# Kernel tuning notes

Measured on AMD Instinct MI355X. Metric: run time of the kernel, lower is better.

The kernel has to match this reference:

```python
import jax, jax.numpy as jnp
import numpy as np

B, WK, HRS = 2048, 52, 8760
DT = 0.125          # Euler step in days (3-hourly), exactly representable
RANGE_PRED = 7      # forecast horizon in days


def setup_inputs() -> dict:
    key = jax.random.key(0)
    k1, k2, k3, k4 = jax.random.split(key, 4)
    # X_in: [B, weeks, 5, 1]; channel 0 = start time in days (same across batch,
    # the torch code reads X_in[0, week, 0, 0]); channels 1..4 = N,P,Z,D init.
    X_in = jax.random.uniform(k1, (B, WK, 5, 1), jnp.float32, 0.1, 3.0)
    t0 = jnp.arange(WK, dtype=jnp.float32) * 7.0
    X_in = X_in.at[:, :, 0, 0].set(jnp.broadcast_to(t0, (B, WK)))
    global_f = jax.random.uniform(k2, (B, HRS), jnp.float32)          # light forcing in [0,1]
    global_m = jax.random.uniform(k3, (B, HRS), jnp.float32) * 0.1    # mixing rate, small
    params_value = jax.random.uniform(k4, (B, 10), jnp.float32, 0.1, 1.0)
    return {"X_in": X_in, "global_f": global_f, "global_m": global_m,
            "params_value": params_value, "dt": DT, "range_pred": RANGE_PRED}


def reference(X_in, global_f, global_m, params_value, dt, range_pred):
    # Fixed multipliers from the torch code
    pv = jnp.asarray([1.0, 2.0, 0.1, 0.05, 0.1, 0.3, 0.6, 0.15, 0.4, 0.1], X_in.dtype)
    Q0, Vm, thr = 8.0, 1.0, 0.01  # Q0 = 4 + 2.5 + 1.5 + 0
    chi, rho, gam, lam, eps, alp, bet, eta, phi, zet = [params_value[:, i][:, None] for i in range(10)]  # [B,1]

    n_steps = int(round(range_pred / dt))      # 56
    stride = int(round(1.0 / dt))              # 8 -> daily sampling of output

    # Hourly forcing gather: same time axis for every batch element (torch uses X_in[0,...])
    t0 = X_in[0, :, 0, 0]                                                     # [W]
    times = t0[:, None] + jnp.arange(n_steps + 1, dtype=X_in.dtype) * dt      # [W, S]
    idx = jnp.round(times * 24.0).astype(jnp.int32)
    f = jnp.take(global_f, idx, axis=1)[:, :, :n_steps]                       # [B, W, T]
    m = jnp.take(global_m, idx, axis=1)[:, :, :n_steps]

    def step(carry, ft_mt):
        N, P, Z, D = carry                      # each [B, W]
        ft, mt = ft_mt
        Pc = jnp.maximum(thr, P)
        Zc = jnp.maximum(thr, Z)
        gN = N / (chi * pv[0] + N)
        zg = rho * pv[1] * (1.0 - jnp.exp(-lam * pv[3] * Pc)) * Zc
        up = Vm * gN * ft * Pc
        Nn = N + dt * (-up + alp * pv[5] * zg + eps * pv[4] * P + gam * pv[2] * Z + phi * pv[8] * D + mt * (Q0 - N))
        Pn = P + dt * (up - zg - eps * pv[4] * P - eta * pv[7] * P - mt * P)
        Zn = Z + dt * (bet * pv[6] * zg - gam * pv[2] * Z - mt * Z)
        Dn = D + dt * (eta * pv[7] * P + (1.0 - alp * pv[5] - bet * pv[6]) * zg - phi * pv[8] * D - zet * pv[9] * D - mt * D)
        new = (Nn, Pn, Zn, Dn)
        return new, jnp.stack(new, axis=0)      # [4, B, W]

    carry0 = (X_in[:, :, 1, 0], X_in[:, :, 2, 0], X_in[:, :, 3, 0], X_in[:, :, 4, 0])
    _, ys = jax.lax.scan(step, carry0, (jnp.moveaxis(f, 2, 0), jnp.moveaxis(m, 2, 0)))  # ys: [T, 4, B, W]
    traj = jnp.concatenate([jnp.stack(carry0, axis=0)[None], ys], axis=0)               # [S, 4, B, W]
    out = jnp.moveaxis(traj, (0, 1), (3, 2))                                            # [B, W, 4, S]
    return out[:, :, :, ::stride]               # daily samples: [B, W, 4, range_pred+1]
```

## Files before the change

kernel.cpp:

```cpp
#include <hip/hip_runtime.h>


typedef float f32x4 __attribute__((ext_vector_type(4)));

#define NPZD_B 2048
#define NPZD_WK 52
#define NPZD_HRS 8760
#define NPZD_NF4 2190
#define NPZD_WSTRIDE 60
#define NPZD_LDSW (NPZD_WK * NPZD_WSTRIDE + 16)

__global__ __launch_bounds__(64, 4) void npzd_kernel(
    const float* __restrict__ X_in,
    const float* __restrict__ gf,
    const float* __restrict__ gm,
    const float* __restrict__ params,
    const float* __restrict__ dt_ptr,
    float* __restrict__ out)
{
    __shared__ __align__(16) float lds_f[NPZD_LDSW];
    __shared__ __align__(16) float lds_m[NPZD_LDSW];

    const int b    = blockIdx.x;
    const int lane = threadIdx.x;

    const float dt = dt_ptr[0];
    const int wc = (lane < NPZD_WK) ? lane : (NPZD_WK - 1);
    const float* xb = X_in + ((size_t)b * NPZD_WK + wc) * 5;
    const float x1 = xb[1], x2 = xb[2], x3 = xb[3], x4 = xb[4];

    const float* pp = params + (size_t)b * 10;
    const float chi   = pp[0];
    const float rho2  = pp[1] * 2.0f;
    const float gam1  = pp[2] * 0.1f;
    const float lam05 = pp[3] * 0.05f;
    const float eps1  = pp[4] * 0.1f;
    const float alp3  = pp[5] * 0.3f;
    const float bet6  = pp[6] * 0.6f;
    const float eta15 = pp[7] * 0.15f;
    const float phi4  = pp[8] * 0.4f;
    const float zet1  = pp[9] * 0.1f;
    const float rem   = 1.0f - alp3 - bet6;

    const f32x4* __restrict__ gf4 = (const f32x4*)(gf + (size_t)b * NPZD_HRS);
    const f32x4* __restrict__ gm4 = (const f32x4*)(gm + (size_t)b * NPZD_HRS);

    #pragma unroll
    for (int pass = 0; pass < 4; ++pass) {
        f32x4 fv[9], mv[9];
        int kk[9];
        #pragma unroll
        for (int c = 0; c < 9; ++c) {
            int k = (pass * 9 + c) * 64 + lane;
            if (k >= NPZD_NF4) k = NPZD_NF4 - 1;
            kk[c] = k;
            fv[c] = gf4[k];
            mv[c] = gm4[k];
        }
        #pragma unroll
        for (int c = 0; c < 9; ++c) {
            const int k = kk[c];
            const float fe[4] = {fv[c].x, fv[c].y, fv[c].z, fv[c].w};
            const float me[4] = {mv[c].x, mv[c].y, mv[c].z, mv[c].w};
            const int rm = k % 3;
            const int e0 = (rm == 0) ? 0 : (3 - rm);
            const int j0 = (4 * k + e0) / 3;
            const int p0 = j0 + 4 * ((j0 * 9363) >> 19);
            lds_f[p0] = fe[e0];
            lds_m[p0] = me[e0];
            if (rm == 0) {
                const int j1 = j0 + 1;
                const int p1 = j1 + 4 * ((j1 * 9363) >> 19);
                lds_f[p1] = fe[3];
                lds_m[p1] = me[3];
            }
        }
    }
    __syncthreads();

    if (lane >= NPZD_WK) return;
    const int w = lane;

    float N = x1, P = x2, Z = x3, D = x4;

    float oN[8], oP[8], oZ[8], oD[8];
    oN[0] = N; oP[0] = P; oZ[0] = Z; oD[0] = D;

    const float* lf = lds_f + w * NPZD_WSTRIDE;
    const float* lm = lds_m + w * NPZD_WSTRIDE;

    #pragma unroll
    for (int g = 0; g < 14; ++g) {
        const f32x4 f4 = *(const f32x4*)(lf + 4 * g);
        const f32x4 m4 = *(const f32x4*)(lm + 4 * g);
        const float fs[4] = {f4.x, f4.y, f4.z, f4.w};
        const float ms[4] = {m4.x, m4.y, m4.z, m4.w};
        #pragma unroll
        for (int q = 0; q < 4; ++q) {
            const float ft = fs[q], mt = ms[q];
            const float Pc = fmaxf(0.01f, P);
            const float Zc = fmaxf(0.01f, Z);
            const float gN = N * __builtin_amdgcn_rcpf(chi + N);
            const float zg = rho2 * (1.0f - __expf(-lam05 * Pc)) * Zc;
            const float up = gN * ft * Pc;
            const float Nn = N + dt * (-up + alp3 * zg + eps1 * P + gam1 * Z + phi4 * D + mt * (8.0f - N));
            const float Pn = P + dt * (up - zg - eps1 * P - eta15 * P - mt * P);
            const float Zn = Z + dt * (bet6 * zg - gam1 * Z - mt * Z);
            const float Dn = D + dt * (eta15 * P + rem * zg - phi4 * D - zet1 * D - mt * D);
            N = Nn; P = Pn; Z = Zn; D = Dn;
        }
        if (g & 1) {
            const int c = (g >> 1) + 1;
            oN[c] = N; oP[c] = P; oZ[c] = Z; oD[c] = D;
        }
    }

    f32x4* o4 = (f32x4*)(out + ((size_t)b * NPZD_WK + w) * 32);
    o4[0] = (f32x4){oN[0], oN[1], oN[2], oN[3]};
    o4[1] = (f32x4){oN[4], oN[5], oN[6], oN[7]};
    o4[2] = (f32x4){oP[0], oP[1], oP[2], oP[3]};
    o4[3] = (f32x4){oP[4], oP[5], oP[6], oP[7]};
    o4[4] = (f32x4){oZ[0], oZ[1], oZ[2], oZ[3]};
    o4[5] = (f32x4){oZ[4], oZ[5], oZ[6], oZ[7]};
    o4[6] = (f32x4){oD[0], oD[1], oD[2], oD[3]};
    o4[7] = (f32x4){oD[4], oD[5], oD[6], oD[7]};
}

extern "C" void kernel_launch(void* const* d_in, const int* in_sizes, int n_in,
                              void* d_out, int out_size, void* d_ws, size_t ws_size,
                              hipStream_t stream) {
    const float* X_in   = (const float*)d_in[0];
    const float* gf     = (const float*)d_in[1];
    const float* gm     = (const float*)d_in[2];
    const float* params = (const float*)d_in[3];
    const float* dt_ptr = (const float*)d_in[4];
    float* out = (float*)d_out;

    npzd_kernel<<<NPZD_B, 64, 0, stream>>>(X_in, gf, gm, params, dt_ptr, out);
}
```

Before: 182.8 us.

## Split batch rows across two blocks and pipeline forcing loads with integration

Each batch element is now handled by two blocks, each covering 26 weeks, which doubles the grid and halves the forcing data each block stages. Within a block, the forcing is loaded in two chunks of half-weeks, and the first chunk is integrated while the second chunk's global loads are in flight. The intent is to shrink LDS use, add parallelism, and hide memory latency behind the serial ODE steps. The cost is more blocks, an extra barrier, and only 26 of 64 lanes doing compute.

```diff
diff --git a/kernel.cpp b/kernel.cpp
--- a/kernel.cpp
+++ b/kernel.cpp
@@ -6,9 +6,11 @@
 #define NPZD_B 2048
 #define NPZD_WK 52
 #define NPZD_HRS 8760
-#define NPZD_NF4 2190
-#define NPZD_WSTRIDE 60
-#define NPZD_LDSW (NPZD_WK * NPZD_WSTRIDE + 16)
+#define NPZD_WKH 26
+#define NPZD_CS 28
+#define NPZD_F4C 21
+#define NPZD_NI 546
+#define NPZD_LDSW (NPZD_WKH * NPZD_CS)
 
 __global__ __launch_bounds__(64, 4) void npzd_kernel(
     const float* __restrict__ X_in,
@@ -21,12 +23,15 @@
     __shared__ __align__(16) float lds_f[NPZD_LDSW];
     __shared__ __align__(16) float lds_m[NPZD_LDSW];
 
-    const int b    = blockIdx.x;
+    const int bid  = blockIdx.x;
+    const int b    = bid >> 1;
+    const int hb   = bid & 1;
     const int lane = threadIdx.x;
 
     const float dt = dt_ptr[0];
-    const int wc = (lane < NPZD_WK) ? lane : (NPZD_WK - 1);
-    const float* xb = X_in + ((size_t)b * NPZD_WK + wc) * 5;
+    const int wl = (lane < NPZD_WKH) ? lane : (NPZD_WKH - 1);
+    const int wg = NPZD_WKH * hb + wl;
+    const float* xb = X_in + ((size_t)b * NPZD_WK + wg) * 5;
     const float x1 = xb[1], x2 = xb[2], x3 = xb[3], x4 = xb[4];
 
     const float* pp = params + (size_t)b * 10;
@@ -45,77 +50,82 @@
     const f32x4* __restrict__ gf4 = (const f32x4*)(gf + (size_t)b * NPZD_HRS);
     const f32x4* __restrict__ gm4 = (const f32x4*)(gm + (size_t)b * NPZD_HRS);
 
+    float N = x1, P = x2, Z = x3, D = x4;
+    float oN[8], oP[8], oZ[8], oD[8];
+    oN[0] = N; oP[0] = P; oZ[0] = Z; oD[0] = D;
+
     #pragma unroll
-    for (int pass = 0; pass < 4; ++pass) {
+    for (int c = 0; c < 2; ++c) {
         f32x4 fv[9], mv[9];
-        int kk[9];
+        int ii[9];
         #pragma unroll
-        for (int c = 0; c < 9; ++c) {
-            int k = (pass * 9 + c) * 64 + lane;
-            if (k >= NPZD_NF4) k = NPZD_NF4 - 1;
-            kk[c] = k;
-            fv[c] = gf4[k];
-            mv[c] = gm4[k];
+        for (int t = 0; t < 9; ++t) {
+            int i = t * 64 + lane;
+            if (i >= NPZD_NI) i = NPZD_NI - 1;
+            ii[t] = i;
+            const int w = (i * 49933) >> 20;
+            const int f = i - 21 * w;
+            const int k = 42 * (NPZD_WKH * hb + w) + NPZD_F4C * c + f;
+            fv[t] = gf4[k];
+            mv[t] = gm4[k];
         }
+
+        if (c) __syncthreads();
+
         #pragma unroll
-        for (int c = 0; c < 9; ++c) {
-            const int k = kk[c];
-            const float fe[4] = {fv[c].x, fv[c].y, fv[c].z, fv[c].w};
-            const float me[4] = {mv[c].x, mv[c].y, mv[c].z, mv[c].w};
-            const int rm = k % 3;
+        for (int t = 0; t < 9; ++t) {
+            const int i = ii[t];
+            const int w = (i * 49933) >> 20;
+            const int f = i - 21 * w;
+            const float fe[4] = {fv[t].x, fv[t].y, fv[t].z, fv[t].w};
+            const float me[4] = {mv[t].x, mv[t].y, mv[t].z, mv[t].w};
+            const int rm = f % 3;
             const int e0 = (rm == 0) ? 0 : (3 - rm);
-            const int j0 = (4 * k + e0) / 3;
-            const int p0 = j0 + 4 * ((j0 * 9363) >> 19);
-            lds_f[p0] = fe[e0];
-            lds_m[p0] = me[e0];
+            const int tp = (4 * f + e0) / 3;
+            const int p  = NPZD_CS * w + tp;
+            lds_f[p] = fe[e0];
+            lds_m[p] = me[e0];
             if (rm == 0) {
-                const int j1 = j0 + 1;
-                const int p1 = j1 + 4 * ((j1 * 9363) >> 19);
-                lds_f[p1] = fe[3];
-                lds_m[p1] = me[3];
+                lds_f[p + 1] = fe[3];
+                lds_m[p + 1] = me[3];
+            }
+        }
+        __syncthreads();
+
+        if (lane < NPZD_WKH) {
+            const float* lf = lds_f + wl * NPZD_CS;
+            const float* lm = lds_m + wl * NPZD_CS;
+            #pragma unroll
+            for (int g = 0; g < 7; ++g) {
+                const f32x4 f4 = *(const f32x4*)(lf + 4 * g);
+                const f32x4 m4 = *(const f32x4*)(lm + 4 * g);
+                const float fs[4] = {f4.x, f4.y, f4.z, f4.w};
+                const float ms[4] = {m4.x, m4.y, m4.z, m4.w};
+                #pragma unroll
+                for (int q = 0; q < 4; ++q) {
+                    const float ft = fs[q], mt = ms[q];
+                    const float Pc = fmaxf(0.01f, P);
+                    const float Zc = fmaxf(0.01f, Z);
+                    const float gN = N * __builtin_amdgcn_rcpf(chi + N);
+                    const float zg = rho2 * (1.0f - __expf(-lam05 * Pc)) * Zc;
+                    const float up = gN * ft * Pc;
+                    const float Nn = N + dt * (-up + alp3 * zg + eps1 * P + gam1 * Z + phi4 * D + mt * (8.0f - N));
+                    const float Pn = P + dt * (up - zg - eps1 * P - eta15 * P - mt * P);
+                    const float Zn = Z + dt * (bet6 * zg - gam1 * Z - mt * Z);
+                    const float Dn = D + dt * (eta15 * P + rem * zg - phi4 * D - zet1 * D - mt * D);
+                    N = Nn; P = Pn; Z = Zn; D = Dn;
+                }
+                const int g14 = 7 * c + g;
+                if (g14 & 1) {
+                    const int co = (g14 >> 1) + 1;
+                    oN[co] = N; oP[co] = P; oZ[co] = Z; oD[co] = D;
+                }
             }
         }
     }
-    __syncthreads();
 
-    if (lane >= NPZD_WK) return;
-    const int w = lane;
-
-    float N = x1, P = x2, Z = x3, D = x4;
-
-    float oN[8], oP[8], oZ[8], oD[8];
-    oN[0] = N; oP[0] = P; oZ[0] = Z; oD[0] = D;
-
-    const float* lf = lds_f + w * NPZD_WSTRIDE;
-    const float* lm = lds_m + w * NPZD_WSTRIDE;
-
-    #pragma unroll
-    for (int g = 0; g < 14; ++g) {
-        const f32x4 f4 = *(const f32x4*)(lf + 4 * g);
-        const f32x4 m4 = *(const f32x4*)(lm + 4 * g);
-        const float fs[4] = {f4.x, f4.y, f4.z, f4.w};
-        const float ms[4] = {m4.x, m4.y, m4.z, m4.w};
-        #pragma unroll
-        for (int q = 0; q < 4; ++q) {
-            const float ft = fs[q], mt = ms[q];
-            const float Pc = fmaxf(0.01f, P);
-            const float Zc = fmaxf(0.01f, Z);
-            const float gN = N * __builtin_amdgcn_rcpf(chi + N);
-            const float zg = rho2 * (1.0f - __expf(-lam05 * Pc)) * Zc;
-            const float up = gN * ft * Pc;
-            const float Nn = N + dt * (-up + alp3 * zg + eps1 * P + gam1 * Z + phi4 * D + mt * (8.0f - N));
-            const float Pn = P + dt * (up - zg - eps1 * P - eta15 * P - mt * P);
-            const float Zn = Z + dt * (bet6 * zg - gam1 * Z - mt * Z);
-            const float Dn = D + dt * (eta15 * P + rem * zg - phi4 * D - zet1 * D - mt * D);
-            N = Nn; P = Pn; Z = Zn; D = Dn;
-        }
-        if (g & 1) {
-            const int c = (g >> 1) + 1;
-            oN[c] = N; oP[c] = P; oZ[c] = Z; oD[c] = D;
-        }
-    }
-
-    f32x4* o4 = (f32x4*)(out + ((size_t)b * NPZD_WK + w) * 32);
+    if (lane >= NPZD_WKH) return;
+    f32x4* o4 = (f32x4*)(out + ((size_t)b * NPZD_WK + wg) * 32);
     o4[0] = (f32x4){oN[0], oN[1], oN[2], oN[3]};
     o4[1] = (f32x4){oN[4], oN[5], oN[6], oN[7]};
     o4[2] = (f32x4){oP[0], oP[1], oP[2], oP[3]};
@@ -136,5 +146,5 @@
     const float* dt_ptr = (const float*)d_in[4];
     float* out = (float*)d_out;
 
-    npzd_kernel<<<NPZD_B, 64, 0, stream>>>(X_in, gf, gm, params, dt_ptr, out);
+    npzd_kernel<<<NPZD_B * 2, 64, 0, stream>>>(X_in, gf, gm, params, dt_ptr, out);
 }
```

New measurement: 189.5 us. 3.7% more time.

## Split NPZD into staging gather kernel and separate integration kernel via workspace

Applied to the files above, without the earlier changes.

Splits the single fused kernel in two. The first kernel uses 256-thread blocks to gather the sampled forcing values through LDS and write them to a workspace in a compact coalesced layout. The second kernel packs four batch elements per 256-thread block and runs the Euler integration, reading forcing from the workspace. The aim is to decouple the bandwidth-bound gather from the latency-bound serial integration so each gets better occupancy, at the cost of an extra global write and read round trip (about 47 MB) and a second launch. The original fused kernel is kept as a fallback when the workspace is too small.

```diff
diff --git a/kernel.cpp b/kernel.cpp
--- a/kernel.cpp
+++ b/kernel.cpp
@@ -9,14 +9,144 @@
 #define NPZD_NF4 2190
 #define NPZD_WSTRIDE 60
 #define NPZD_LDSW (NPZD_WK * NPZD_WSTRIDE + 16)
-
-__global__ __launch_bounds__(64, 4) void npzd_kernel(
-    const float* __restrict__ X_in,
+#define NPZD_OPB 728
+
+__global__ __launch_bounds__(256) void npzd_stage(
     const float* __restrict__ gf,
     const float* __restrict__ gm,
+    f32x4* __restrict__ fc,
+    f32x4* __restrict__ mc)
+{
+    __shared__ __align__(16) float lds_f[NPZD_LDSW];
+    __shared__ __align__(16) float lds_m[NPZD_LDSW];
+
+    const int b   = blockIdx.x;
+    const int tid = threadIdx.x;
+
+    const f32x4* __restrict__ gf4 = (const f32x4*)(gf + (size_t)b * NPZD_HRS);
+    const f32x4* __restrict__ gm4 = (const f32x4*)(gm + (size_t)b * NPZD_HRS);
+
+    f32x4 fv[9], mv[9];
+    int kk[9];
+    #pragma unroll
+    for (int i = 0; i < 9; ++i) {
+        int k = i * 256 + tid;
+        if (k >= NPZD_NF4) k = NPZD_NF4 - 1;
+        kk[i] = k;
+        fv[i] = gf4[k];
+        mv[i] = gm4[k];
+    }
+
+    #pragma unroll
+    for (int i = 0; i < 9; ++i) {
+        const int k = kk[i];
+        const float fe[4] = {fv[i].x, fv[i].y, fv[i].z, fv[i].w};
+        const float me[4] = {mv[i].x, mv[i].y, mv[i].z, mv[i].w};
+        const int rm = k % 3;
+        const int e0 = (rm == 0) ? 0 : (3 - rm);
+        const int j0 = (4 * k + e0) / 3;
+        const int p0 = j0 + 4 * ((j0 * 9363) >> 19);
+        lds_f[p0] = fe[e0];
+        lds_m[p0] = me[e0];
+        if (rm == 0) {
+            const int j1 = j0 + 1;
+            const int p1 = j1 + 4 * ((j1 * 9363) >> 19);
+            lds_f[p1] = fe[3];
+            lds_m[p1] = me[3];
+        }
+    }
+    __syncthreads();
+
+    #pragma unroll
+    for (int i = 0; i < 3; ++i) {
+        const int o = tid + 256 * i;
+        if (o < NPZD_OPB) {
+            const int g = (o * 5042) >> 18;
+            const int w = o - 52 * g;
+            const int src = 60 * w + 4 * g;
+            fc[(size_t)b * NPZD_OPB + o] = *(const f32x4*)(lds_f + src);
+            mc[(size_t)b * NPZD_OPB + o] = *(const f32x4*)(lds_m + src);
+        }
+    }
+}
+
+__global__ __launch_bounds__(256) void npzd_integrate(
+    const float* __restrict__ X_in,
+    const f32x4* __restrict__ fc,
+    const f32x4* __restrict__ mc,
     const float* __restrict__ params,
     const float* __restrict__ dt_ptr,
     float* __restrict__ out)
+{
+    const int wave = threadIdx.x >> 6;
+    const int lane = threadIdx.x & 63;
+    const int b    = blockIdx.x * 4 + wave;
+    const int wl   = (lane < NPZD_WK) ? lane : (NPZD_WK - 1);
+
+    const float dt = dt_ptr[0];
+    const float* xb = X_in + ((size_t)b * NPZD_WK + wl) * 5;
+    float N = xb[1], P = xb[2], Z = xb[3], D = xb[4];
+
+    const float* pp = params + (size_t)b * 10;
+    const float chi   = pp[0];
+    const float rho2  = pp[1] * 2.0f;
+    const float gam1  = pp[2] * 0.1f;
+    const float lam05 = pp[3] * 0.05f;
+    const float eps1  = pp[4] * 0.1f;
+    const float alp3  = pp[5] * 0.3f;
+    const float bet6  = pp[6] * 0.6f;
+    const float eta15 = pp[7] * 0.15f;
+    const float phi4  = pp[8] * 0.4f;
+    const float zet1  = pp[9] * 0.1f;
+    const float rem   = 1.0f - alp3 - bet6;
+
+    float oN[8], oP[8], oZ[8], oD[8];
+    oN[0] = N; oP[0] = P; oZ[0] = Z; oD[0] = D;
+
+    const size_t base = (size_t)b * NPZD_OPB + wl;
+
+    #pragma unroll
+    for (int g = 0; g < 14; ++g) {
+        const f32x4 f4 = fc[base + 52 * g];
+        const f32x4 m4 = mc[base + 52 * g];
+        const float fs[4] = {f4.x, f4.y, f4.z, f4.w};
+        const float ms[4] = {m4.x, m4.y, m4.z, m4.w};
+        #pragma unroll
+        for (int q = 0; q < 4; ++q) {
+            const float ft = fs[q], mt = ms[q];
+            const float Pc = fmaxf(0.01f, P);
+            const float Zc = fmaxf(0.01f, Z);
+            const float gN = N * __builtin_amdgcn_rcpf(chi + N);
+            const float zg = rho2 * (1.0f - __expf(-lam05 * Pc)) * Zc;
+            const float up = gN * ft * Pc;
+            const float Nn = N + dt * (-up + alp3 * zg + eps1 * P + gam1 * Z + phi4 * D + mt * (8.0f - N));
+            const float Pn = P + dt * (up - zg - eps1 * P - eta15 * P - mt * P);
+            const float Zn = Z + dt * (bet6 * zg - gam1 * Z - mt * Z);
+            const float Dn = D + dt * (eta15 * P + rem * zg - phi4 * D - zet1 * D - mt * D);
+            N = Nn; P = Pn; Z = Zn; D = Dn;
+        }
+        if (g & 1) {
+            const int c = (g >> 1) + 1;
+            oN[c] = N; oP[c] = P; oZ[c] = Z; oD[c] = D;
+        }
+    }
+
+    if (lane >= NPZD_WK) return;
+    f32x4* o4 = (f32x4*)(out + ((size_t)b * NPZD_WK + wl) * 32);
+    o4[0] = (f32x4){oN[0], oN[1], oN[2], oN[3]};
+    o4[1] = (f32x4){oN[4], oN[5], oN[6], oN[7]};
+    o4[2] = (f32x4){oP[0], oP[1], oP[2], oP[3]};
+    o4[3] = (f32x4){oP[4], oP[5], oP[6], oP[7]};
+    o4[4] = (f32x4){oZ[0], oZ[1], oZ[2], oZ[3]};
+    o4[5] = (f32x4){oZ[4], oZ[5], oZ[6], oZ[7]};
+    o4[6] = (f32x4){oD[0], oD[1], oD[2], oD[3]};
+    o4[7] = (f32x4){oD[4], oD[5], oD[6], oD[7]};
+}
+
+__global__ __launch_bounds__(64, 4) void npzd_mono(
+    const float* __restrict__ X_in, const float* __restrict__ gf,
+    const float* __restrict__ gm, const float* __restrict__ params,
+    const float* __restrict__ dt_ptr, float* __restrict__ out)
 {
     __shared__ __align__(16) float lds_f[NPZD_LDSW];
     __shared__ __align__(16) float lds_m[NPZD_LDSW];
@@ -80,15 +210,11 @@
 
     if (lane >= NPZD_WK) return;
     const int w = lane;
-
     float N = x1, P = x2, Z = x3, D = x4;
-
     float oN[8], oP[8], oZ[8], oD[8];
     oN[0] = N; oP[0] = P; oZ[0] = Z; oD[0] = D;
-
     const float* lf = lds_f + w * NPZD_WSTRIDE;
     const float* lm = lds_m + w * NPZD_WSTRIDE;
-
     #pragma unroll
     for (int g = 0; g < 14; ++g) {
         const f32x4 f4 = *(const f32x4*)(lf + 4 * g);
@@ -114,7 +240,6 @@
             oN[c] = N; oP[c] = P; oZ[c] = Z; oD[c] = D;
         }
     }
-
     f32x4* o4 = (f32x4*)(out + ((size_t)b * NPZD_WK + w) * 32);
     o4[0] = (f32x4){oN[0], oN[1], oN[2], oN[3]};
     o4[1] = (f32x4){oN[4], oN[5], oN[6], oN[7]};
@@ -136,5 +261,13 @@
     const float* dt_ptr = (const float*)d_in[4];
     float* out = (float*)d_out;
 
-    npzd_kernel<<<NPZD_B, 64, 0, stream>>>(X_in, gf, gm, params, dt_ptr, out);
-}
+    const size_t need = (size_t)2 * NPZD_B * NPZD_OPB * sizeof(f32x4);
+    if (ws_size >= need && d_ws != nullptr) {
+        f32x4* fc = (f32x4*)d_ws;
+        f32x4* mc = fc + (size_t)NPZD_B * NPZD_OPB;
+        npzd_stage<<<NPZD_B, 256, 0, stream>>>(gf, gm, fc, mc);
+        npzd_integrate<<<NPZD_B / 4, 256, 0, stream>>>(X_in, fc, mc, params, dt_ptr, out);
+    } else {
+        npzd_mono<<<NPZD_B, 64, 0, stream>>>(X_in, gf, gm, params, dt_ptr, out);
+    }
+}
```

Result: slower. 192.9 us (+5.5%).

## Stream forcing directly from global memory per lane with register double-buffering

Applied to the files above, without the earlier changes.

Drops the cooperative LDS staging of the forcing arrays and the block barrier. Each lane now loads its own week's 3-hourly forcing samples straight from global memory as float4 vectors, taking every third hourly sample, and prefetches the next chunk into a second register set while the current chunk is integrated. This removes the shared-memory scatter and the __syncthreads, and frees LDS so more blocks can reside. In exchange each lane reads three times the data it uses with strided, less coalesced loads. Launch bounds are relaxed from 4 to 2 to allow more registers for the double buffers.

```diff
diff --git a/kernel.cpp b/kernel.cpp
--- a/kernel.cpp
+++ b/kernel.cpp
@@ -6,11 +6,8 @@
 #define NPZD_B 2048
 #define NPZD_WK 52
 #define NPZD_HRS 8760
-#define NPZD_NF4 2190
-#define NPZD_WSTRIDE 60
-#define NPZD_LDSW (NPZD_WK * NPZD_WSTRIDE + 16)
 
-__global__ __launch_bounds__(64, 4) void npzd_kernel(
+__global__ __launch_bounds__(64, 2) void npzd_kernel(
     const float* __restrict__ X_in,
     const float* __restrict__ gf,
     const float* __restrict__ gm,
@@ -18,16 +15,20 @@
     const float* __restrict__ dt_ptr,
     float* __restrict__ out)
 {
-    __shared__ __align__(16) float lds_f[NPZD_LDSW];
-    __shared__ __align__(16) float lds_m[NPZD_LDSW];
-
     const int b    = blockIdx.x;
     const int lane = threadIdx.x;
+    const int w    = (lane < NPZD_WK) ? lane : (NPZD_WK - 1);
+
+    const f32x4* __restrict__ gfw = (const f32x4*)(gf + (size_t)b * NPZD_HRS) + 42 * w;
+    const f32x4* __restrict__ gmw = (const f32x4*)(gm + (size_t)b * NPZD_HRS) + 42 * w;
+
+    f32x4 fA0 = gfw[0], fA1 = gfw[1], fA2 = gfw[2];
+    f32x4 mA0 = gmw[0], mA1 = gmw[1], mA2 = gmw[2];
+    f32x4 fB0, fB1, fB2, mB0, mB1, mB2;
 
     const float dt = dt_ptr[0];
-    const int wc = (lane < NPZD_WK) ? lane : (NPZD_WK - 1);
-    const float* xb = X_in + ((size_t)b * NPZD_WK + wc) * 5;
-    const float x1 = xb[1], x2 = xb[2], x3 = xb[3], x4 = xb[4];
+    const float* xb = X_in + ((size_t)b * NPZD_WK + w) * 5;
+    float N = xb[1], P = xb[2], Z = xb[3], D = xb[4];
 
     const float* pp = params + (size_t)b * 10;
     const float chi   = pp[0];
@@ -42,59 +43,34 @@
     const float zet1  = pp[9] * 0.1f;
     const float rem   = 1.0f - alp3 - bet6;
 
-    const f32x4* __restrict__ gf4 = (const f32x4*)(gf + (size_t)b * NPZD_HRS);
-    const f32x4* __restrict__ gm4 = (const f32x4*)(gm + (size_t)b * NPZD_HRS);
-
-    #pragma unroll
-    for (int pass = 0; pass < 4; ++pass) {
-        f32x4 fv[9], mv[9];
-        int kk[9];
-        #pragma unroll
-        for (int c = 0; c < 9; ++c) {
-            int k = (pass * 9 + c) * 64 + lane;
-            if (k >= NPZD_NF4) k = NPZD_NF4 - 1;
-            kk[c] = k;
-            fv[c] = gf4[k];
-            mv[c] = gm4[k];
-        }
-        #pragma unroll
-        for (int c = 0; c < 9; ++c) {
-            const int k = kk[c];
-            const float fe[4] = {fv[c].x, fv[c].y, fv[c].z, fv[c].w};
-            const float me[4] = {mv[c].x, mv[c].y, mv[c].z, mv[c].w};
-            const int rm = k % 3;
-            const int e0 = (rm == 0) ? 0 : (3 - rm);
-            const int j0 = (4 * k + e0) / 3;
-            const int p0 = j0 + 4 * ((j0 * 9363) >> 19);
-            lds_f[p0] = fe[e0];
-            lds_m[p0] = me[e0];
-            if (rm == 0) {
-                const int j1 = j0 + 1;
-                const int p1 = j1 + 4 * ((j1 * 9363) >> 19);
-                lds_f[p1] = fe[3];
-                lds_m[p1] = me[3];
-            }
-        }
-    }
-    __syncthreads();
-
-    if (lane >= NPZD_WK) return;
-    const int w = lane;
-
-    float N = x1, P = x2, Z = x3, D = x4;
-
     float oN[8], oP[8], oZ[8], oD[8];
     oN[0] = N; oP[0] = P; oZ[0] = Z; oD[0] = D;
 
-    const float* lf = lds_f + w * NPZD_WSTRIDE;
-    const float* lm = lds_m + w * NPZD_WSTRIDE;
-
     #pragma unroll
     for (int g = 0; g < 14; ++g) {
-        const f32x4 f4 = *(const f32x4*)(lf + 4 * g);
-        const f32x4 m4 = *(const f32x4*)(lm + 4 * g);
-        const float fs[4] = {f4.x, f4.y, f4.z, f4.w};
-        const float ms[4] = {m4.x, m4.y, m4.z, m4.w};
+        const bool even = (g & 1) == 0;
+
+        if (g < 13) {
+            const f32x4* pf = gfw + 3 * (g + 1);
+            const f32x4* pm = gmw + 3 * (g + 1);
+            if (even) {
+                fB0 = pf[0]; fB1 = pf[1]; fB2 = pf[2];
+                mB0 = pm[0]; mB1 = pm[1]; mB2 = pm[2];
+            } else {
+                fA0 = pf[0]; fA1 = pf[1]; fA2 = pf[2];
+                mA0 = pm[0]; mA1 = pm[1]; mA2 = pm[2];
+            }
+        }
+
+        const f32x4 cf0 = even ? fA0 : fB0;
+        const f32x4 cf1 = even ? fA1 : fB1;
+        const f32x4 cf2 = even ? fA2 : fB2;
+        const f32x4 cm0 = even ? mA0 : mB0;
+        const f32x4 cm1 = even ? mA1 : mB1;
+        const f32x4 cm2 = even ? mA2 : mB2;
+        const float fs[4] = {cf0.x, cf0.w, cf1.z, cf2.y};
+        const float ms[4] = {cm0.x, cm0.w, cm1.z, cm2.y};
+
         #pragma unroll
         for (int q = 0; q < 4; ++q) {
             const float ft = fs[q], mt = ms[q];
@@ -115,6 +91,7 @@
         }
     }
 
+    if (lane >= NPZD_WK) return;
     f32x4* o4 = (f32x4*)(out + ((size_t)b * NPZD_WK + w) * 32);
     o4[0] = (f32x4){oN[0], oN[1], oN[2], oN[3]};
     o4[1] = (f32x4){oN[4], oN[5], oN[6], oN[7]};
```

Measured after the change: 208.2 us. 1.14x slower.
